# Performance work log

Hardware: AMD Instinct MI355X
Metric: run time of the kernel (lower is better)

## Reference

```python
import jax, jax.numpy as jnp
import numpy as np

VEC_SIZE = 256
N_VECS = 8
N_CHOICES = 2048
BATCH = 2048
EPS = 1e-6
NAND_BIAS = 3.0


def setup_inputs() -> dict:
    key = jax.random.key(0)
    k1, k2 = jax.random.split(key)
    query = jax.random.normal(k1, (BATCH, N_VECS * VEC_SIZE), dtype=jnp.float32)
    weight = jax.random.normal(k2, (N_CHOICES, VEC_SIZE * N_VECS), dtype=jnp.float32)
    # init code overwrites the randn nand_weight with ones + nand_bias
    nand_weight = jnp.full((N_CHOICES, N_VECS), 1.0 + NAND_BIAS, dtype=jnp.float32)
    return {"query": query, "weight": weight, "nand_weight": nand_weight}


def reference(query, weight, nand_weight):
    # [B, n_vecs, vec_size] and [C, n_vecs, vec_size]
    q = query.reshape(-1, N_VECS, VEC_SIZE)
    w = weight.reshape(-1, N_VECS, VEC_SIZE)
    # torch.cosine_similarity clamps each norm to eps
    qn = q / jnp.maximum(jnp.linalg.norm(q, axis=-1, keepdims=True), EPS)
    wn = w / jnp.maximum(jnp.linalg.norm(w, axis=-1, keepdims=True), EPS)
    # broadcast cosine sim expressed as batched matmul: [B, C, n_vecs]
    cos_sim = jnp.einsum('bnd,cnd->bcn', qn, wn)
    cos_sim = jax.nn.leaky_relu(cos_sim)  # slope 0.01, matches F.leaky_relu default
    nw = jax.nn.sigmoid(nand_weight)[None]  # [1, C, n_vecs]
    interpolated = nw * cos_sim + (1.0 - nw) * (1.0 - cos_sim)
    return jnp.prod(interpolated, axis=2)  # [B, C]
```

## Files before the change

kernel.cpp:

```cpp
#include <hip/hip_runtime.h>
#include <math.h>
#include <stdint.h>

#define BATCH    2048
#define NCHOICES 2048
#define NV       8
#define VS       256
#define KTOT     2048

typedef unsigned short u16;
typedef __attribute__((ext_vector_type(8))) short    bf16x8;
typedef __attribute__((ext_vector_type(8))) u16      u16x8;
typedef __attribute__((ext_vector_type(4))) float    f32x4;

__device__ __forceinline__ u16 f2bf_rne(float x) {
    unsigned u = __float_as_uint(x);
    return (u16)((u + 0x7FFFu + ((u >> 16) & 1u)) >> 16);
}

__global__ __launch_bounds__(256) void prep_convert(
    const float* __restrict__ Q, const float* __restrict__ W,
    const float* __restrict__ NWT,
    u16* __restrict__ Qh, u16* __restrict__ Ql,
    u16* __restrict__ Wh, u16* __restrict__ Wl,
    float* __restrict__ rq, float* __restrict__ rw, float* __restrict__ snw)
{
    const int row = blockIdx.x;
    const int t   = threadIdx.x;
    const int n   = t >> 5;
    const int l   = t & 31;

    const float* src; u16 *dh, *dl; float* dst;
    if (row < BATCH) {
        src = Q + (size_t)row * KTOT;
        dh = Qh + (size_t)row * KTOT; dl = Ql + (size_t)row * KTOT;
        dst = rq + (size_t)row * NV;
    } else {
        src = W + (size_t)(row - BATCH) * KTOT;
        dh = Wh + (size_t)(row - BATCH) * KTOT; dl = Wl + (size_t)(row - BATCH) * KTOT;
        dst = rw + (size_t)(row - BATCH) * NV;
    }

    const int idx = n * VS + l * 8;
    float4 x0 = *(const float4*)(src + idx);
    float4 x1 = *(const float4*)(src + idx + 4);
    float xs[8] = {x0.x, x0.y, x0.z, x0.w, x1.x, x1.y, x1.z, x1.w};

    u16x8 hv, lv;
    float s = 0.0f;
    #pragma unroll
    for (int j = 0; j < 8; ++j) {
        u16 h = f2bf_rne(xs[j]);
        float hf = __uint_as_float(((unsigned)h) << 16);
        hv[j] = h;
        lv[j] = f2bf_rne(xs[j] - hf);
        s = fmaf(xs[j], xs[j], s);
    }
    *(u16x8*)(dh + idx) = hv;
    *(u16x8*)(dl + idx) = lv;

    #pragma unroll
    for (int m = 1; m < 32; m <<= 1) s += __shfl_xor(s, m, 64);
    if (l == 0) dst[n] = 1.0f / fmaxf(sqrtf(s), 1e-6f);

    if (row >= BATCH && t < NV) {
        const int c = row - BATCH;
        float x = NWT[(size_t)c * NV + t];
        snw[(size_t)c * NV + t] = 1.0f / (1.0f + expf(-x));
    }
}

__device__ __forceinline__ void gload16(const void* g, void* l) {
    __builtin_amdgcn_global_load_lds(
        (__attribute__((address_space(1))) void*)(uintptr_t)g,
        (__attribute__((address_space(3))) void*)(uint32_t)(uintptr_t)l,
        16, 0, 0);
}

#define RD16(dst, va, OFF) \
    asm volatile("ds_read_b128 %0, %1 offset:" OFF : "=v"(dst) : "v"(va))

__global__ __launch_bounds__(256, 2) void nand_mfma2b(
    const u16* __restrict__ Qh, const u16* __restrict__ Ql,
    const u16* __restrict__ Wh, const u16* __restrict__ Wl,
    const float* __restrict__ rq, const float* __restrict__ rw,
    const float* __restrict__ snw, float* __restrict__ part)
{
    __shared__ __align__(16) u16 L[2][16384];

    const int tid  = threadIdx.x;
    const int lane = tid & 63;
    const int wave = tid >> 6;

    const int f    = blockIdx.x + 16 * blockIdx.y + 256 * blockIdx.z;
    const int virt = (f & 7) * 64 + (f >> 3);
    const int bx   = virt & 15;
    const int by   = (virt >> 4) & 15;
    const int z    = virt >> 8;

    const int wr   = (wave >> 1) * 64;
    const int wc   = (wave & 1) * 64;
    const int bm0  = by * 128;
    const int bn0  = bx * 128;
    const int kb   = z * 1024;

    const int fr = lane & 15;
    const int gi = lane >> 4;
    const int ri = gi * 4;

    const int lr = lane >> 2;
    const int sw = 8 * ((lane & 3) ^ ((lane >> 3) & 3));
    const int r0 = wave * 32 + lr;
    const int r1 = r0 + 16;

    const u16* sAh0 = Qh + (size_t)(bm0 + r0) * KTOT + kb + sw;
    const u16* sAh1 = Qh + (size_t)(bm0 + r1) * KTOT + kb + sw;
    const u16* sAl0 = Ql + (size_t)(bm0 + r0) * KTOT + kb + sw;
    const u16* sAl1 = Ql + (size_t)(bm0 + r1) * KTOT + kb + sw;
    const u16* sBh0 = Wh + (size_t)(bn0 + r0) * KTOT + kb + sw;
    const u16* sBh1 = Wh + (size_t)(bn0 + r1) * KTOT + kb + sw;
    const u16* sBl0 = Wl + (size_t)(bn0 + r0) * KTOT + kb + sw;
    const u16* sBl1 = Wl + (size_t)(bn0 + r1) * KTOT + kb + sw;

    #define STAGE(B, T) do { u16* Lb_ = &L[B][0]; const int ko = (T) * 32;   \
        gload16(sAh0 + ko, Lb_ + wave * 1024);                               \
        gload16(sAh1 + ko, Lb_ + wave * 1024 + 512);                         \
        gload16(sAl0 + ko, Lb_ + 4096  + wave * 1024);                       \
        gload16(sAl1 + ko, Lb_ + 4096  + wave * 1024 + 512);                 \
        gload16(sBh0 + ko, Lb_ + 8192  + wave * 1024);                       \
        gload16(sBh1 + ko, Lb_ + 8192  + wave * 1024 + 512);                 \
        gload16(sBl0 + ko, Lb_ + 12288 + wave * 1024);                       \
        gload16(sBl1 + ko, Lb_ + 12288 + wave * 1024 + 512);                 \
    } while (0)

    const uint32_t ldsBase = (uint32_t)(uintptr_t)&L[0][0];
    const uint32_t swz16   = (uint32_t)((gi ^ ((fr >> 1) & 3)) * 16);
    const uint32_t vbaseA  = ldsBase + (uint32_t)((wr + fr) * 64) + swz16;
    const uint32_t vbaseB  = ldsBase + 16384u + (uint32_t)((wc + fr) * 64) + swz16;

    #define MM(M, N) do {                                                   \
        acc[M][N] = __builtin_amdgcn_mfma_f32_16x16x32_bf16(ah[M], bh[N], acc[M][N], 0, 0, 0); \
        acc[M][N] = __builtin_amdgcn_mfma_f32_16x16x32_bf16(ah[M], bl[N], acc[M][N], 0, 0, 0); \
        acc[M][N] = __builtin_amdgcn_mfma_f32_16x16x32_bf16(al[M], bh[N], acc[M][N], 0, 0, 0); } while (0)

    f32x4 prod[4][4];
    #pragma unroll
    for (int m = 0; m < 4; ++m)
        #pragma unroll
        for (int n = 0; n < 4; ++n) prod[m][n] = (f32x4){1.f, 1.f, 1.f, 1.f};

    STAGE(0, 0);
    asm volatile("s_waitcnt vmcnt(0)");
    __builtin_amdgcn_s_barrier();

    int buf = 0;

    #pragma unroll 1
    for (int cc = 0; cc < 4; ++cc) {
        const int chunk = z * 4 + cc;

        f32x4 acc[4][4];
        #pragma unroll
        for (int m = 0; m < 4; ++m)
            #pragma unroll
            for (int n = 0; n < 4; ++n) acc[m][n] = (f32x4){0.f, 0.f, 0.f, 0.f};

        #pragma unroll 1
        for (int t8 = 0; t8 < 8; ++t8) {
            const int t = cc * 8 + t8;

            if (t + 1 < 32) STAGE(buf ^ 1, t + 1);
            __builtin_amdgcn_sched_barrier(0);

            const uint32_t vaA = vbaseA + ((uint32_t)buf << 15);
            const uint32_t vaB = vbaseB + ((uint32_t)buf << 15);

            bf16x8 ah[4], al[4], bh[4], bl[4];
            RD16(ah[0], vaA, "0");     RD16(bh[0], vaB, "0");
            RD16(al[0], vaA, "8192");  RD16(bl[0], vaB, "8192");
            RD16(ah[1], vaA, "1024");  RD16(bh[1], vaB, "1024");
            RD16(al[1], vaA, "9216");  RD16(bl[1], vaB, "9216");
            RD16(ah[2], vaA, "2048");  RD16(bh[2], vaB, "2048");
            RD16(al[2], vaA, "10240"); RD16(bl[2], vaB, "10240");
            RD16(ah[3], vaA, "3072");  RD16(bh[3], vaB, "3072");
            RD16(al[3], vaA, "11264"); RD16(bl[3], vaB, "11264");

            __builtin_amdgcn_s_setprio(1);
            asm volatile("s_waitcnt lgkmcnt(12)");
            __builtin_amdgcn_sched_barrier(0);
            MM(0, 0);
            asm volatile("s_waitcnt lgkmcnt(8)");
            __builtin_amdgcn_sched_barrier(0);
            MM(0, 1); MM(1, 0); MM(1, 1);
            asm volatile("s_waitcnt lgkmcnt(4)");
            __builtin_amdgcn_sched_barrier(0);
            MM(0, 2); MM(1, 2); MM(2, 0); MM(2, 1); MM(2, 2);
            asm volatile("s_waitcnt lgkmcnt(0)");
            __builtin_amdgcn_sched_barrier(0);
            MM(0, 3); MM(1, 3); MM(2, 3); MM(3, 0); MM(3, 1); MM(3, 2); MM(3, 3);
            __builtin_amdgcn_s_setprio(0);

            asm volatile("s_waitcnt vmcnt(0)");
            __builtin_amdgcn_s_barrier();
            buf ^= 1;
        }

        float rwv[4], vv[4], uu[4];
        #pragma unroll
        for (int n = 0; n < 4; ++n) {
            const int col = bn0 + wc + n * 16 + fr;
            rwv[n] = rw[(size_t)col * NV + chunk];
            float s = snw[(size_t)col * NV + chunk];
            vv[n] = 2.0f * s - 1.0f;
            uu[n] = 1.0f - s;
        }
        #pragma unroll
        for (int m = 0; m < 4; ++m) {
            #pragma unroll
            for (int i = 0; i < 4; ++i) {
                const float rqv =
                    rq[(size_t)(bm0 + wr + m * 16 + ri + i) * NV + chunk];
                #pragma unroll
                for (int n = 0; n < 4; ++n) {
                    float cosv = acc[m][n][i] * rqv * rwv[n];
                    float Lk = fmaxf(cosv, 0.01f * cosv);
                    prod[m][n][i] *= fmaf(Lk, vv[n], uu[n]);
                }
            }
        }
    }

    float* P = part + (size_t)z * BATCH * NCHOICES;
    #pragma unroll
    for (int m = 0; m < 4; ++m)
        #pragma unroll
        for (int i = 0; i < 4; ++i) {
            const int row = bm0 + wr + m * 16 + ri + i;
            float* pr = P + (size_t)row * NCHOICES + bn0 + wc + fr;
            #pragma unroll
            for (int n = 0; n < 4; ++n) pr[n * 16] = prod[m][n][i];
        }

    #undef STAGE
    #undef MM
}

__global__ __launch_bounds__(256) void combine_kernel(
    const float* __restrict__ p, float* __restrict__ out)
{
    const size_t NN = (size_t)BATCH * NCHOICES;
    size_t i = ((size_t)blockIdx.x * 256 + threadIdx.x) * 4;
    float4 a = *(const float4*)(p + i);
    float4 b = *(const float4*)(p + NN + i);
    float4 o;
    o.x = a.x * b.x;
    o.y = a.y * b.y;
    o.z = a.z * b.z;
    o.w = a.w * b.w;
    *(float4*)(out + i) = o;
}

__global__ __launch_bounds__(256) void prep_kernel(
    const float* __restrict__ Q, const float* __restrict__ W,
    const float* __restrict__ NWT,
    float* __restrict__ rq, float* __restrict__ rw, float* __restrict__ snw)
{
    const int row = blockIdx.x;
    const int t   = threadIdx.x;
    const int n   = t >> 5;
    const int l   = t & 31;

    const float* src; float* dst;
    if (row < BATCH) { src = Q + (size_t)row * KTOT; dst = rq + (size_t)row * NV; }
    else { src = W + (size_t)(row - BATCH) * KTOT; dst = rw + (size_t)(row - BATCH) * NV; }

    const float* v = src + n * VS + l * 8;
    float4 a = *(const float4*)(v);
    float4 b = *(const float4*)(v + 4);
    float s = a.x*a.x + a.y*a.y + a.z*a.z + a.w*a.w
            + b.x*b.x + b.y*b.y + b.z*b.z + b.w*b.w;
    #pragma unroll
    for (int m = 1; m < 32; m <<= 1) s += __shfl_xor(s, m, 64);
    if (l == 0) dst[n] = 1.0f / fmaxf(sqrtf(s), 1e-6f);
    if (row >= BATCH && t < NV) {
        const int c = row - BATCH;
        float x = NWT[(size_t)c * NV + t];
        snw[(size_t)c * NV + t] = 1.0f / (1.0f + expf(-x));
    }
}

__global__ __launch_bounds__(256, 2) void nand_gemm(
    const float* __restrict__ Q, const float* __restrict__ W,
    const float* __restrict__ rq, const float* __restrict__ rw,
    const float* __restrict__ snw, float* __restrict__ out)
{
    __shared__ __align__(16) float As[16][128 + 4];
    __shared__ __align__(16) float Bs[16][128 + 4];
    __shared__ __align__(16) float rqs[128];
    __shared__ __align__(16) float rws[128];
    __shared__ __align__(16) float sns[128];

    const int tid = threadIdx.x;
    const int tx  = tid & 15;
    const int ty  = tid >> 4;
    const int bm0 = blockIdx.y * 128;
    const int bn0 = blockIdx.x * 128;
    const int lr  = tid >> 2;
    const int lk  = (tid & 3) * 4;

    float prod[8][8];
    #pragma unroll
    for (int i = 0; i < 8; ++i)
        #pragma unroll
        for (int j = 0; j < 8; ++j) prod[i][j] = 1.0f;

    for (int n = 0; n < NV; ++n) {
        float acc[8][8];
        #pragma unroll
        for (int i = 0; i < 8; ++i)
            #pragma unroll
            for (int j = 0; j < 8; ++j) acc[i][j] = 0.0f;

        #pragma unroll 1
        for (int kt = 0; kt < VS / 16; ++kt) {
            const int k0 = n * VS + kt * 16;
            __syncthreads();
            {
                const float* qrow = Q + (size_t)(bm0 + lr) * KTOT + k0 + lk;
                float4 a0 = *(const float4*)(qrow);
                float4 a1 = *(const float4*)(qrow + (size_t)64 * KTOT);
                As[lk + 0][lr] = a0.x; As[lk + 1][lr] = a0.y;
                As[lk + 2][lr] = a0.z; As[lk + 3][lr] = a0.w;
                As[lk + 0][64 + lr] = a1.x; As[lk + 1][64 + lr] = a1.y;
                As[lk + 2][64 + lr] = a1.z; As[lk + 3][64 + lr] = a1.w;

                const float* wrow = W + (size_t)(bn0 + lr) * KTOT + k0 + lk;
                float4 b0 = *(const float4*)(wrow);
                float4 b1 = *(const float4*)(wrow + (size_t)64 * KTOT);
                Bs[lk + 0][lr] = b0.x; Bs[lk + 1][lr] = b0.y;
                Bs[lk + 2][lr] = b0.z; Bs[lk + 3][lr] = b0.w;
                Bs[lk + 0][64 + lr] = b1.x; Bs[lk + 1][64 + lr] = b1.y;
                Bs[lk + 2][64 + lr] = b1.z; Bs[lk + 3][64 + lr] = b1.w;
            }
            if (kt == 0) {
                for (int i = tid; i < 3 * 128; i += 256) {
                    if (i < 128)      rqs[i]       = rq[(size_t)(bm0 + i) * NV + n];
                    else if (i < 256) rws[i - 128] = rw[(size_t)(bn0 + i - 128) * NV + n];
                    else              sns[i - 256] = snw[(size_t)(bn0 + i - 256) * NV + n];
                }
            }
            __syncthreads();

            #pragma unroll
            for (int kk = 0; kk < 16; ++kk) {
                float4 a0 = *(const float4*)&As[kk][ty * 4];
                float4 a1 = *(const float4*)&As[kk][64 + ty * 4];
                float4 b0 = *(const float4*)&Bs[kk][tx * 4];
                float4 b1 = *(const float4*)&Bs[kk][64 + tx * 4];
                float ar[8] = {a0.x, a0.y, a0.z, a0.w, a1.x, a1.y, a1.z, a1.w};
                float br[8] = {b0.x, b0.y, b0.z, b0.w, b1.x, b1.y, b1.z, b1.w};
                #pragma unroll
                for (int i = 0; i < 8; ++i)
                    #pragma unroll
                    for (int j = 0; j < 8; ++j)
                        acc[i][j] = fmaf(ar[i], br[j], acc[i][j]);
            }
        }

        float rwv[8], uu[8], vv[8];
        #pragma unroll
        for (int j = 0; j < 8; ++j) {
            int cc = (j < 4) ? (tx * 4 + j) : (64 + tx * 4 + (j - 4));
            rwv[j] = rws[cc];
            float s = sns[cc];
            uu[j] = 1.0f - s;
            vv[j] = 2.0f * s - 1.0f;
        }
        #pragma unroll
        for (int i = 0; i < 8; ++i) {
            int r = (i < 4) ? (ty * 4 + i) : (64 + ty * 4 + (i - 4));
            float rqv = rqs[r];
            #pragma unroll
            for (int j = 0; j < 8; ++j) {
                float cosv = acc[i][j] * rqv * rwv[j];
                float Lk = fmaxf(cosv, 0.01f * cosv);
                prod[i][j] *= fmaf(Lk, vv[j], uu[j]);
            }
        }
    }

    #pragma unroll
    for (int i = 0; i < 8; ++i) {
        int r = (i < 4) ? (ty * 4 + i) : (64 + ty * 4 + (i - 4));
        float* orow = out + (size_t)(bm0 + r) * NCHOICES + bn0;
        float4 o0 = {prod[i][0], prod[i][1], prod[i][2], prod[i][3]};
        float4 o1 = {prod[i][4], prod[i][5], prod[i][6], prod[i][7]};
        *(float4*)(orow + tx * 4)      = o0;
        *(float4*)(orow + 64 + tx * 4) = o1;
    }
}

extern "C" void kernel_launch(void* const* d_in, const int* in_sizes, int n_in,
                              void* d_out, int out_size, void* d_ws, size_t ws_size,
                              hipStream_t stream)
{
    const float* Q   = (const float*)d_in[0];
    const float* W   = (const float*)d_in[1];
    const float* NWT = (const float*)d_in[2];
    float* out = (float*)d_out;

    char* w = (char*)d_ws;
    float* rq  = (float*)w; w += (size_t)BATCH    * NV * 4;
    float* rwn = (float*)w; w += (size_t)NCHOICES * NV * 4;
    float* snw = (float*)w; w += (size_t)NCHOICES * NV * 4;
    u16* Qh = (u16*)w; w += (size_t)BATCH * KTOT * 2;
    u16* Ql = (u16*)w; w += (size_t)BATCH * KTOT * 2;
    u16* Wh = (u16*)w; w += (size_t)NCHOICES * KTOT * 2;
    u16* Wl = (u16*)w; w += (size_t)NCHOICES * KTOT * 2;
    float* part = (float*)w; w += (size_t)2 * BATCH * NCHOICES * 4;
    const size_t needed = (size_t)(w - (char*)d_ws);

    if (ws_size >= needed) {
        prep_convert<<<BATCH + NCHOICES, 256, 0, stream>>>(
            Q, W, NWT, Qh, Ql, Wh, Wl, rq, rwn, snw);
        dim3 grid(NCHOICES / 128, BATCH / 128, 2);
        nand_mfma2b<<<grid, 256, 0, stream>>>(Qh, Ql, Wh, Wl, rq, rwn, snw, part);
        combine_kernel<<<(BATCH * NCHOICES / 4) / 256, 256, 0, stream>>>(part, out);
    } else {
        prep_kernel<<<BATCH + NCHOICES, 256, 0, stream>>>(Q, W, NWT, rq, rwn, snw);
        dim3 grid(NCHOICES / 128, BATCH / 128);
        nand_gemm<<<grid, 256, 0, stream>>>(Q, W, rq, rwn, snw, out);
    }
}
```

Before: 84.41 us.

## Prenormalize inputs and pipeline GEMM with 4-stage LDS ring and register double-buffering

The prep kernel now normalizes each 256-vector before splitting it into bf16 hi/lo parts, so the GEMM epilogue no longer loads or multiplies rq/rw norms. The main kernel replaces the 2-buffer loop with a 4-deep LDS ring that prefetches three tiles ahead, plus double-buffered register fragments read in groups interleaved with MFMA blocks. The sigmoid constants are fetched inline with global_load_dword and the chunk epilogue is fused into the pipeline. The cost is occupancy: launch bounds drop to 1 block per CU because LDS use rises to 128KB and register pressure grows, and the hand-tuned waitcnt counts are fragile.

```diff
diff --git a/kernel.cpp b/kernel.cpp
--- a/kernel.cpp
+++ b/kernel.cpp
@@ -23,22 +23,20 @@
     const float* __restrict__ NWT,
     u16* __restrict__ Qh, u16* __restrict__ Ql,
     u16* __restrict__ Wh, u16* __restrict__ Wl,
-    float* __restrict__ rq, float* __restrict__ rw, float* __restrict__ snw)
+    float* __restrict__ snw)
 {
     const int row = blockIdx.x;
     const int t   = threadIdx.x;
     const int n   = t >> 5;
     const int l   = t & 31;
 
-    const float* src; u16 *dh, *dl; float* dst;
+    const float* src; u16 *dh, *dl;
     if (row < BATCH) {
         src = Q + (size_t)row * KTOT;
         dh = Qh + (size_t)row * KTOT; dl = Ql + (size_t)row * KTOT;
-        dst = rq + (size_t)row * NV;
     } else {
         src = W + (size_t)(row - BATCH) * KTOT;
         dh = Wh + (size_t)(row - BATCH) * KTOT; dl = Wl + (size_t)(row - BATCH) * KTOT;
-        dst = rw + (size_t)(row - BATCH) * NV;
     }
 
     const int idx = n * VS + l * 8;
@@ -46,22 +44,24 @@
     float4 x1 = *(const float4*)(src + idx + 4);
     float xs[8] = {x0.x, x0.y, x0.z, x0.w, x1.x, x1.y, x1.z, x1.w};
 
+    float s = 0.0f;
+    #pragma unroll
+    for (int j = 0; j < 8; ++j) s = fmaf(xs[j], xs[j], s);
+    #pragma unroll
+    for (int m = 1; m < 32; m <<= 1) s += __shfl_xor(s, m, 64);
+    const float rn = 1.0f / fmaxf(sqrtf(s), 1e-6f);
+
     u16x8 hv, lv;
-    float s = 0.0f;
     #pragma unroll
     for (int j = 0; j < 8; ++j) {
-        u16 h = f2bf_rne(xs[j]);
+        float xn = xs[j] * rn;
+        u16 h = f2bf_rne(xn);
         float hf = __uint_as_float(((unsigned)h) << 16);
         hv[j] = h;
-        lv[j] = f2bf_rne(xs[j] - hf);
-        s = fmaf(xs[j], xs[j], s);
+        lv[j] = f2bf_rne(xn - hf);
     }
     *(u16x8*)(dh + idx) = hv;
     *(u16x8*)(dl + idx) = lv;
-
-    #pragma unroll
-    for (int m = 1; m < 32; m <<= 1) s += __shfl_xor(s, m, 64);
-    if (l == 0) dst[n] = 1.0f / fmaxf(sqrtf(s), 1e-6f);
 
     if (row >= BATCH && t < NV) {
         const int c = row - BATCH;
@@ -80,13 +80,33 @@
 #define RD16(dst, va, OFF) \
     asm volatile("ds_read_b128 %0, %1 offset:" OFF : "=v"(dst) : "v"(va))
 
-__global__ __launch_bounds__(256, 2) void nand_mfma2b(
+#define GLD_F32(dst, p) \
+    asm volatile("global_load_dword %0, %1, off" : "=v"(dst) : "v"(p))
+
+__device__ __forceinline__ void chunk_epi(f32x4 (&acc)[4][4], f32x4 (&prod)[4][4],
+                                          float sn0, float sn1, float sn2, float sn3)
+{
+    float vvv[4] = {2.f*sn0-1.f, 2.f*sn1-1.f, 2.f*sn2-1.f, 2.f*sn3-1.f};
+    float uuu[4] = {1.f-sn0, 1.f-sn1, 1.f-sn2, 1.f-sn3};
+    #pragma unroll
+    for (int m = 0; m < 4; ++m)
+        #pragma unroll
+        for (int i = 0; i < 4; ++i)
+            #pragma unroll
+            for (int n = 0; n < 4; ++n) {
+                float cosv = acc[m][n][i];
+                float Lk = fmaxf(cosv, 0.01f * cosv);
+                prod[m][n][i] *= fmaf(Lk, vvv[n], uuu[n]);
+                acc[m][n][i] = 0.f;
+            }
+}
+
+__global__ __launch_bounds__(256, 1) void nand_pipe(
     const u16* __restrict__ Qh, const u16* __restrict__ Ql,
     const u16* __restrict__ Wh, const u16* __restrict__ Wl,
-    const float* __restrict__ rq, const float* __restrict__ rw,
     const float* __restrict__ snw, float* __restrict__ part)
 {
-    __shared__ __align__(16) u16 L[2][16384];
+    __shared__ __align__(16) u16 L[4][16384];
 
     const int tid  = threadIdx.x;
     const int lane = tid & 63;
@@ -98,11 +118,11 @@
     const int by   = (virt >> 4) & 15;
     const int z    = virt >> 8;
 
-    const int wr   = (wave >> 1) * 64;
-    const int wc   = (wave & 1) * 64;
-    const int bm0  = by * 128;
-    const int bn0  = bx * 128;
-    const int kb   = z * 1024;
+    const int wr  = (wave >> 1) * 64;
+    const int wc  = (wave & 1) * 64;
+    const int bm0 = by * 128;
+    const int bn0 = bx * 128;
+    const int kb  = z * 1024;
 
     const int fr = lane & 15;
     const int gi = lane >> 4;
@@ -138,96 +158,96 @@
     const uint32_t vbaseA  = ldsBase + (uint32_t)((wr + fr) * 64) + swz16;
     const uint32_t vbaseB  = ldsBase + 16384u + (uint32_t)((wc + fr) * 64) + swz16;
 
-    #define MM(M, N) do {                                                   \
-        acc[M][N] = __builtin_amdgcn_mfma_f32_16x16x32_bf16(ah[M], bh[N], acc[M][N], 0, 0, 0); \
-        acc[M][N] = __builtin_amdgcn_mfma_f32_16x16x32_bf16(ah[M], bl[N], acc[M][N], 0, 0, 0); \
-        acc[M][N] = __builtin_amdgcn_mfma_f32_16x16x32_bf16(al[M], bh[N], acc[M][N], 0, 0, 0); } while (0)
-
-    f32x4 prod[4][4];
+    #define RD_G1(S, BUFN) do {                                             \
+        const uint32_t vaA = vbaseA + (BUFN) * 32768u;                      \
+        const uint32_t vaB = vbaseB + (BUFN) * 32768u;                      \
+        RD16(ah##S[0], vaA, "0");    RD16(bh##S[0], vaB, "0");              \
+        RD16(al##S[0], vaA, "8192"); RD16(bl##S[0], vaB, "8192");           \
+        RD16(ah##S[1], vaA, "1024"); RD16(bh##S[1], vaB, "1024");           \
+        RD16(al##S[1], vaA, "9216"); RD16(bl##S[1], vaB, "9216"); } while (0)
+    #define RD_G2(S, BUFN) do {                                             \
+        const uint32_t vaB = vbaseB + (BUFN) * 32768u;                      \
+        RD16(bh##S[2], vaB, "2048");  RD16(bh##S[3], vaB, "3072");          \
+        RD16(bl##S[2], vaB, "10240"); RD16(bl##S[3], vaB, "11264"); } while (0)
+    #define RD_G3(S, BUFN) do {                                             \
+        const uint32_t vaA = vbaseA + (BUFN) * 32768u;                      \
+        RD16(ah##S[2], vaA, "2048");  RD16(ah##S[3], vaA, "3072");          \
+        RD16(al##S[2], vaA, "10240"); RD16(al##S[3], vaA, "11264"); } while (0)
+
+    #define MM3(S, M, N) do {                                               \
+        acc[M][N] = __builtin_amdgcn_mfma_f32_16x16x32_bf16(ah##S[M], bh##S[N], acc[M][N], 0, 0, 0); \
+        acc[M][N] = __builtin_amdgcn_mfma_f32_16x16x32_bf16(ah##S[M], bl##S[N], acc[M][N], 0, 0, 0); \
+        acc[M][N] = __builtin_amdgcn_mfma_f32_16x16x32_bf16(al##S[M], bh##S[N], acc[M][N], 0, 0, 0); } while (0)
+
+    #define TILE(U, KT0, CS, NS, VMS, LGS, DOREAD, DOSTAGE, DOCONST) do {   \
+        asm volatile("s_waitcnt vmcnt(" VMS ")");                           \
+        __builtin_amdgcn_s_barrier();                                       \
+        if (DOREAD) RD_G1(NS, ((U) + 1) & 3);                               \
+        asm volatile("s_waitcnt lgkmcnt(" LGS ")");                         \
+        __builtin_amdgcn_sched_barrier(0);                                  \
+        MM3(CS,0,0); MM3(CS,0,1); MM3(CS,1,0); MM3(CS,1,1);                 \
+        __builtin_amdgcn_sched_barrier(0);                                  \
+        if (DOREAD) RD_G2(NS, ((U) + 1) & 3);                               \
+        if (DOCONST) { GLD_F32(sn0, snwP);       GLD_F32(sn1, snwP + 128);  \
+                       GLD_F32(sn2, snwP + 256); GLD_F32(sn3, snwP + 384); }\
+        if (DOSTAGE) STAGE(((U) + 3) & 3, (KT0) + (U) + 3);                 \
+        __builtin_amdgcn_sched_barrier(0);                                  \
+        MM3(CS,0,2); MM3(CS,0,3); MM3(CS,1,2); MM3(CS,1,3);                 \
+        __builtin_amdgcn_sched_barrier(0);                                  \
+        if (DOREAD) RD_G3(NS, ((U) + 1) & 3);                               \
+        __builtin_amdgcn_sched_barrier(0);                                  \
+        MM3(CS,2,2); MM3(CS,2,3); MM3(CS,3,2); MM3(CS,3,3);                 \
+        MM3(CS,2,0); MM3(CS,2,1); MM3(CS,3,0); MM3(CS,3,1);                 \
+    } while (0)
+
+    bf16x8 ahA[4], alA[4], bhA[4], blA[4];
+    bf16x8 ahB[4], alB[4], bhB[4], blB[4];
+    f32x4 acc[4][4], prod[4][4];
+    float sn0, sn1, sn2, sn3;
     #pragma unroll
     for (int m = 0; m < 4; ++m)
         #pragma unroll
-        for (int n = 0; n < 4; ++n) prod[m][n] = (f32x4){1.f, 1.f, 1.f, 1.f};
-
-    STAGE(0, 0);
-    asm volatile("s_waitcnt vmcnt(0)");
+        for (int n = 0; n < 4; ++n) {
+            acc[m][n]  = (f32x4){0.f, 0.f, 0.f, 0.f};
+            prod[m][n] = (f32x4){1.f, 1.f, 1.f, 1.f};
+        }
+
+    const float* snwBase = snw + (size_t)(bn0 + wc + fr) * NV + z * 4;
+
+    STAGE(0, 0); STAGE(1, 1); STAGE(2, 2);
+    asm volatile("s_waitcnt vmcnt(16)");
     __builtin_amdgcn_s_barrier();
-
-    int buf = 0;
+    RD_G1(A, 0); RD_G2(A, 0); RD_G3(A, 0);
 
     #pragma unroll 1
-    for (int cc = 0; cc < 4; ++cc) {
-        const int chunk = z * 4 + cc;
-
-        f32x4 acc[4][4];
-        #pragma unroll
-        for (int m = 0; m < 4; ++m)
-            #pragma unroll
-            for (int n = 0; n < 4; ++n) acc[m][n] = (f32x4){0.f, 0.f, 0.f, 0.f};
-
-        #pragma unroll 1
-        for (int t8 = 0; t8 < 8; ++t8) {
-            const int t = cc * 8 + t8;
-
-            if (t + 1 < 32) STAGE(buf ^ 1, t + 1);
-            __builtin_amdgcn_sched_barrier(0);
-
-            const uint32_t vaA = vbaseA + ((uint32_t)buf << 15);
-            const uint32_t vaB = vbaseB + ((uint32_t)buf << 15);
-
-            bf16x8 ah[4], al[4], bh[4], bl[4];
-            RD16(ah[0], vaA, "0");     RD16(bh[0], vaB, "0");
-            RD16(al[0], vaA, "8192");  RD16(bl[0], vaB, "8192");
-            RD16(ah[1], vaA, "1024");  RD16(bh[1], vaB, "1024");
-            RD16(al[1], vaA, "9216");  RD16(bl[1], vaB, "9216");
-            RD16(ah[2], vaA, "2048");  RD16(bh[2], vaB, "2048");
-            RD16(al[2], vaA, "10240"); RD16(bl[2], vaB, "10240");
-            RD16(ah[3], vaA, "3072");  RD16(bh[3], vaB, "3072");
-            RD16(al[3], vaA, "11264"); RD16(bl[3], vaB, "11264");
-
-            __builtin_amdgcn_s_setprio(1);
-            asm volatile("s_waitcnt lgkmcnt(12)");
-            __builtin_amdgcn_sched_barrier(0);
-            MM(0, 0);
-            asm volatile("s_waitcnt lgkmcnt(8)");
-            __builtin_amdgcn_sched_barrier(0);
-            MM(0, 1); MM(1, 0); MM(1, 1);
-            asm volatile("s_waitcnt lgkmcnt(4)");
-            __builtin_amdgcn_sched_barrier(0);
-            MM(0, 2); MM(1, 2); MM(2, 0); MM(2, 1); MM(2, 2);
-            asm volatile("s_waitcnt lgkmcnt(0)");
-            __builtin_amdgcn_sched_barrier(0);
-            MM(0, 3); MM(1, 3); MM(2, 3); MM(3, 0); MM(3, 1); MM(3, 2); MM(3, 3);
-            __builtin_amdgcn_s_setprio(0);
-
-            asm volatile("s_waitcnt vmcnt(0)");
-            __builtin_amdgcn_s_barrier();
-            buf ^= 1;
-        }
-
-        float rwv[4], vv[4], uu[4];
-        #pragma unroll
-        for (int n = 0; n < 4; ++n) {
-            const int col = bn0 + wc + n * 16 + fr;
-            rwv[n] = rw[(size_t)col * NV + chunk];
-            float s = snw[(size_t)col * NV + chunk];
-            vv[n] = 2.0f * s - 1.0f;
-            uu[n] = 1.0f - s;
-        }
-        #pragma unroll
-        for (int m = 0; m < 4; ++m) {
-            #pragma unroll
-            for (int i = 0; i < 4; ++i) {
-                const float rqv =
-                    rq[(size_t)(bm0 + wr + m * 16 + ri + i) * NV + chunk];
-                #pragma unroll
-                for (int n = 0; n < 4; ++n) {
-                    float cosv = acc[m][n][i] * rqv * rwv[n];
-                    float Lk = fmaxf(cosv, 0.01f * cosv);
-                    prod[m][n][i] *= fmaf(Lk, vv[n], uu[n]);
-                }
-            }
-        }
+    for (int cc = 0; cc < 3; ++cc) {
+        const int kt0 = cc * 8;
+        const float* snwP = snwBase + cc;
+        TILE(0, kt0, A, B, "8", "8", 1, 1, 0);
+        TILE(1, kt0, B, A, "8", "8", 1, 1, 0);
+        TILE(2, kt0, A, B, "8", "8", 1, 1, 0);
+        TILE(3, kt0, B, A, "8", "8", 1, 1, 0);
+        TILE(4, kt0, A, B, "8", "8", 1, 1, 0);
+        TILE(5, kt0, B, A, "8", "8", 1, 1, 0);
+        TILE(6, kt0, A, B, "8", "8", 1, 1, 0);
+        TILE(7, kt0, B, A, "8", "8", 1, 1, 1);
+        asm volatile("s_waitcnt vmcnt(8)");
+        __builtin_amdgcn_sched_barrier(0);
+        chunk_epi(acc, prod, sn0, sn1, sn2, sn3);
+    }
+    {
+        const float* snwP = snwBase + 3;
+        TILE(0, 24, A, B, "8", "8", 1, 1, 0);
+        TILE(1, 24, B, A, "8", "8", 1, 1, 0);
+        TILE(2, 24, A, B, "8", "8", 1, 1, 0);
+        TILE(3, 24, B, A, "8", "8", 1, 1, 0);
+        TILE(4, 24, A, B, "8", "8", 1, 1, 0);
+        TILE(5, 24, B, A, "8", "8", 1, 0, 0);
+        TILE(6, 24, A, B, "0", "8", 1, 0, 0);
+        TILE(7, 24, B, A, "0", "0", 0, 0, 1);
+        asm volatile("s_waitcnt vmcnt(0)");
+        __builtin_amdgcn_sched_barrier(0);
+        chunk_epi(acc, prod, sn0, sn1, sn2, sn3);
     }
 
     float* P = part + (size_t)z * BATCH * NCHOICES;
@@ -242,7 +262,11 @@
         }
 
     #undef STAGE
-    #undef MM
+    #undef RD_G1
+    #undef RD_G2
+    #undef RD_G3
+    #undef MM3
+    #undef TILE
 }
 
 __global__ __launch_bounds__(256) void combine_kernel(
@@ -422,9 +446,9 @@
 
     if (ws_size >= needed) {
         prep_convert<<<BATCH + NCHOICES, 256, 0, stream>>>(
-            Q, W, NWT, Qh, Ql, Wh, Wl, rq, rwn, snw);
+            Q, W, NWT, Qh, Ql, Wh, Wl, snw);
         dim3 grid(NCHOICES / 128, BATCH / 128, 2);
-        nand_mfma2b<<<grid, 256, 0, stream>>>(Qh, Ql, Wh, Wl, rq, rwn, snw, part);
+        nand_pipe<<<grid, 256, 0, stream>>>(Qh, Ql, Wh, Wl, snw, part);
         combine_kernel<<<(BATCH * NCHOICES / 4) / 256, 256, 0, stream>>>(part, out);
     } else {
         prep_kernel<<<BATCH + NCHOICES, 256, 0, stream>>>(Q, W, NWT, rq, rwn, snw);
```

New measurement: 84.89 us. Within noise of the previous version (+0.6%).

## Pre-normalize inputs before bf16 split and reorder MFMA passes by operand

Applied to the files above, without the earlier changes.

The conversion kernel now computes each sub-vector's norm first and scales the values before splitting them into bf16 hi/lo parts. The GEMM epilogue therefore no longer loads rq/rw or multiplies by them. The MFMA loop is reorganized into three full passes (hi*hi, lo*hi, hi*lo) with LDS reads ordered so the first pass needs only the hi fragments, which lets reads overlap compute more cleanly. The changed sched_barrier placement alters the schedule, and pre-normalizing shifts where rounding happens.

```diff
diff --git a/kernel.cpp b/kernel.cpp
--- a/kernel.cpp
+++ b/kernel.cpp
@@ -23,22 +23,20 @@
     const float* __restrict__ NWT,
     u16* __restrict__ Qh, u16* __restrict__ Ql,
     u16* __restrict__ Wh, u16* __restrict__ Wl,
-    float* __restrict__ rq, float* __restrict__ rw, float* __restrict__ snw)
+    float* __restrict__ snw)
 {
     const int row = blockIdx.x;
     const int t   = threadIdx.x;
     const int n   = t >> 5;
     const int l   = t & 31;
 
-    const float* src; u16 *dh, *dl; float* dst;
+    const float* src; u16 *dh, *dl;
     if (row < BATCH) {
         src = Q + (size_t)row * KTOT;
         dh = Qh + (size_t)row * KTOT; dl = Ql + (size_t)row * KTOT;
-        dst = rq + (size_t)row * NV;
     } else {
         src = W + (size_t)(row - BATCH) * KTOT;
         dh = Wh + (size_t)(row - BATCH) * KTOT; dl = Wl + (size_t)(row - BATCH) * KTOT;
-        dst = rw + (size_t)(row - BATCH) * NV;
     }
 
     const int idx = n * VS + l * 8;
@@ -46,22 +44,24 @@
     float4 x1 = *(const float4*)(src + idx + 4);
     float xs[8] = {x0.x, x0.y, x0.z, x0.w, x1.x, x1.y, x1.z, x1.w};
 
+    float s = 0.0f;
+    #pragma unroll
+    for (int j = 0; j < 8; ++j) s = fmaf(xs[j], xs[j], s);
+    #pragma unroll
+    for (int m = 1; m < 32; m <<= 1) s += __shfl_xor(s, m, 64);
+    const float rn = 1.0f / fmaxf(sqrtf(s), 1e-6f);
+
     u16x8 hv, lv;
-    float s = 0.0f;
     #pragma unroll
     for (int j = 0; j < 8; ++j) {
-        u16 h = f2bf_rne(xs[j]);
+        float xn = xs[j] * rn;
+        u16 h = f2bf_rne(xn);
         float hf = __uint_as_float(((unsigned)h) << 16);
         hv[j] = h;
-        lv[j] = f2bf_rne(xs[j] - hf);
-        s = fmaf(xs[j], xs[j], s);
+        lv[j] = f2bf_rne(xn - hf);
     }
     *(u16x8*)(dh + idx) = hv;
     *(u16x8*)(dl + idx) = lv;
-
-    #pragma unroll
-    for (int m = 1; m < 32; m <<= 1) s += __shfl_xor(s, m, 64);
-    if (l == 0) dst[n] = 1.0f / fmaxf(sqrtf(s), 1e-6f);
 
     if (row >= BATCH && t < NV) {
         const int c = row - BATCH;
@@ -80,10 +80,9 @@
 #define RD16(dst, va, OFF) \
     asm volatile("ds_read_b128 %0, %1 offset:" OFF : "=v"(dst) : "v"(va))
 
-__global__ __launch_bounds__(256, 2) void nand_mfma2b(
+__global__ __launch_bounds__(256, 2) void nand_mfma9(
     const u16* __restrict__ Qh, const u16* __restrict__ Ql,
     const u16* __restrict__ Wh, const u16* __restrict__ Wl,
-    const float* __restrict__ rq, const float* __restrict__ rw,
     const float* __restrict__ snw, float* __restrict__ part)
 {
     __shared__ __align__(16) u16 L[2][16384];
@@ -98,15 +97,14 @@
     const int by   = (virt >> 4) & 15;
     const int z    = virt >> 8;
 
-    const int wr   = (wave >> 1) * 64;
-    const int wc   = (wave & 1) * 64;
-    const int bm0  = by * 128;
-    const int bn0  = bx * 128;
-    const int kb   = z * 1024;
+    const int wr  = (wave >> 1) * 64;
+    const int wc  = (wave & 1) * 64;
+    const int bm0 = by * 128;
+    const int bn0 = bx * 128;
+    const int kb  = z * 1024;
 
     const int fr = lane & 15;
     const int gi = lane >> 4;
-    const int ri = gi * 4;
 
     const int lr = lane >> 2;
     const int sw = 8 * ((lane & 3) ^ ((lane >> 3) & 3));
@@ -138,10 +136,14 @@
     const uint32_t vbaseA  = ldsBase + (uint32_t)((wr + fr) * 64) + swz16;
     const uint32_t vbaseB  = ldsBase + 16384u + (uint32_t)((wc + fr) * 64) + swz16;
 
-    #define MM(M, N) do {                                                   \
-        acc[M][N] = __builtin_amdgcn_mfma_f32_16x16x32_bf16(ah[M], bh[N], acc[M][N], 0, 0, 0); \
-        acc[M][N] = __builtin_amdgcn_mfma_f32_16x16x32_bf16(ah[M], bl[N], acc[M][N], 0, 0, 0); \
-        acc[M][N] = __builtin_amdgcn_mfma_f32_16x16x32_bf16(al[M], bh[N], acc[M][N], 0, 0, 0); } while (0)
+    #define MF(AR, BR, M, N) \
+        acc[M][N] = __builtin_amdgcn_mfma_f32_16x16x32_bf16(AR[M], BR[N], acc[M][N], 0, 0, 0)
+    #define PASS(AR, BR) do {                                                \
+        MF(AR, BR, 0, 0); MF(AR, BR, 0, 1); MF(AR, BR, 0, 2); MF(AR, BR, 0, 3); \
+        MF(AR, BR, 1, 0); MF(AR, BR, 1, 1); MF(AR, BR, 1, 2); MF(AR, BR, 1, 3); \
+        MF(AR, BR, 2, 0); MF(AR, BR, 2, 1); MF(AR, BR, 2, 2); MF(AR, BR, 2, 3); \
+        MF(AR, BR, 3, 0); MF(AR, BR, 3, 1); MF(AR, BR, 3, 2); MF(AR, BR, 3, 3); \
+    } while (0)
 
     f32x4 prod[4][4];
     #pragma unroll
@@ -170,34 +172,32 @@
             const int t = cc * 8 + t8;
 
             if (t + 1 < 32) STAGE(buf ^ 1, t + 1);
-            __builtin_amdgcn_sched_barrier(0);
 
             const uint32_t vaA = vbaseA + ((uint32_t)buf << 15);
             const uint32_t vaB = vbaseB + ((uint32_t)buf << 15);
 
             bf16x8 ah[4], al[4], bh[4], bl[4];
             RD16(ah[0], vaA, "0");     RD16(bh[0], vaB, "0");
-            RD16(al[0], vaA, "8192");  RD16(bl[0], vaB, "8192");
             RD16(ah[1], vaA, "1024");  RD16(bh[1], vaB, "1024");
-            RD16(al[1], vaA, "9216");  RD16(bl[1], vaB, "9216");
             RD16(ah[2], vaA, "2048");  RD16(bh[2], vaB, "2048");
-            RD16(al[2], vaA, "10240"); RD16(bl[2], vaB, "10240");
             RD16(ah[3], vaA, "3072");  RD16(bh[3], vaB, "3072");
-            RD16(al[3], vaA, "11264"); RD16(bl[3], vaB, "11264");
+            RD16(al[0], vaA, "8192");  RD16(al[1], vaA, "9216");
+            RD16(al[2], vaA, "10240"); RD16(al[3], vaA, "11264");
+            RD16(bl[0], vaB, "8192");  RD16(bl[1], vaB, "9216");
+            RD16(bl[2], vaB, "10240"); RD16(bl[3], vaB, "11264");
 
             __builtin_amdgcn_s_setprio(1);
-            asm volatile("s_waitcnt lgkmcnt(12)");
-            __builtin_amdgcn_sched_barrier(0);
-            MM(0, 0);
             asm volatile("s_waitcnt lgkmcnt(8)");
             __builtin_amdgcn_sched_barrier(0);
-            MM(0, 1); MM(1, 0); MM(1, 1);
+            PASS(ah, bh);
+            __builtin_amdgcn_sched_barrier(0);
             asm volatile("s_waitcnt lgkmcnt(4)");
             __builtin_amdgcn_sched_barrier(0);
-            MM(0, 2); MM(1, 2); MM(2, 0); MM(2, 1); MM(2, 2);
+            PASS(al, bh);
+            __builtin_amdgcn_sched_barrier(0);
             asm volatile("s_waitcnt lgkmcnt(0)");
             __builtin_amdgcn_sched_barrier(0);
-            MM(0, 3); MM(1, 3); MM(2, 3); MM(3, 0); MM(3, 1); MM(3, 2); MM(3, 3);
+            PASS(ah, bl);
             __builtin_amdgcn_s_setprio(0);
 
             asm volatile("s_waitcnt vmcnt(0)");
@@ -205,31 +205,27 @@
             buf ^= 1;
         }
 
-        float rwv[4], vv[4], uu[4];
+        float vv[4], uu[4];
         #pragma unroll
         for (int n = 0; n < 4; ++n) {
             const int col = bn0 + wc + n * 16 + fr;
-            rwv[n] = rw[(size_t)col * NV + chunk];
             float s = snw[(size_t)col * NV + chunk];
             vv[n] = 2.0f * s - 1.0f;
             uu[n] = 1.0f - s;
         }
         #pragma unroll
-        for (int m = 0; m < 4; ++m) {
-            #pragma unroll
-            for (int i = 0; i < 4; ++i) {
-                const float rqv =
-                    rq[(size_t)(bm0 + wr + m * 16 + ri + i) * NV + chunk];
+        for (int m = 0; m < 4; ++m)
+            #pragma unroll
+            for (int i = 0; i < 4; ++i)
                 #pragma unroll
                 for (int n = 0; n < 4; ++n) {
-                    float cosv = acc[m][n][i] * rqv * rwv[n];
+                    float cosv = acc[m][n][i];
                     float Lk = fmaxf(cosv, 0.01f * cosv);
                     prod[m][n][i] *= fmaf(Lk, vv[n], uu[n]);
                 }
-            }
-        }
-    }
-
+    }
+
+    const int ri = gi * 4;
     float* P = part + (size_t)z * BATCH * NCHOICES;
     #pragma unroll
     for (int m = 0; m < 4; ++m)
@@ -242,7 +238,8 @@
         }
 
     #undef STAGE
-    #undef MM
+    #undef MF
+    #undef PASS
 }
 
 __global__ __launch_bounds__(256) void combine_kernel(
@@ -422,9 +419,9 @@
 
     if (ws_size >= needed) {
         prep_convert<<<BATCH + NCHOICES, 256, 0, stream>>>(
-            Q, W, NWT, Qh, Ql, Wh, Wl, rq, rwn, snw);
+            Q, W, NWT, Qh, Ql, Wh, Wl, snw);
         dim3 grid(NCHOICES / 128, BATCH / 128, 2);
-        nand_mfma2b<<<grid, 256, 0, stream>>>(Qh, Ql, Wh, Wl, rq, rwn, snw, part);
+        nand_mfma9<<<grid, 256, 0, stream>>>(Qh, Ql, Wh, Wl, snw, part);
         combine_kernel<<<(BATCH * NCHOICES / 4) / 256, 256, 0, stream>>>(part, out);
     } else {
         prep_kernel<<<BATCH + NCHOICES, 256, 0, stream>>>(Q, W, NWT, rq, rwn, snw);
```

Measured after the change: 77.74 us. -7.9%, faster.
